# Kernel tuning notes

Measured on AMD Instinct MI355X. Metric: run time of the kernel, lower is better.

## Reference

```python
import jax, jax.numpy as jnp
import numpy as np

B, N, D, H, E, K = 8, 1024, 768, 12, 4, 9
PAD = (K - 1) // 2


def _ln(x, g, b, eps=1e-5):
    m = jnp.mean(x, -1, keepdims=True)
    v = jnp.var(x, -1, keepdims=True)
    return (x - m) * jax.lax.rsqrt(v + eps) * g + b


def setup_inputs() -> dict:
    key = jax.random.key(0)
    ks = jax.random.split(key, 12)
    w = lambda k, s: jax.random.normal(k, s, jnp.float32) * 0.02
    return {
        "x": jax.random.normal(ks[0], (B, N, D), jnp.float32),
        "ff1_ln_g": jnp.ones(D), "ff1_ln_b": jnp.zeros(D),
        "ff1_w1": w(ks[1], (D, E * D)), "ff1_b1": jnp.zeros(E * D),
        "ff1_w2": w(ks[2], (E * D, D)), "ff1_b2": jnp.zeros(D),
        "attn_ln_g": jnp.ones(D), "attn_ln_b": jnp.zeros(D),
        "qkv_w": w(ks[3], (D, 3 * D)), "qkv_b": jnp.zeros(3 * D),
        "proj_w": w(ks[4], (D, D)), "proj_b": jnp.zeros(D),
        "rel_table": w(ks[5], (2 * N - 1, H)),
        "conv_ln_g": jnp.ones(D), "conv_ln_b": jnp.zeros(D),
        "pwin_w": w(ks[6], (2 * D, D)), "pwin_b": jnp.zeros(2 * D),
        "dw_w": w(ks[7], (D, 1, K)), "dw_b": jnp.zeros(D),
        "bn_g": jnp.ones(D), "bn_b": jnp.zeros(D),
        "pwout_w": w(ks[8], (D, D)), "pwout_b": jnp.zeros(D),
        "ff2_ln_g": jnp.ones(D), "ff2_ln_b": jnp.zeros(D),
        "ff2_w1": w(ks[9], (D, E * D)), "ff2_b1": jnp.zeros(E * D),
        "ff2_w2": w(ks[10], (E * D, D)), "ff2_b2": jnp.zeros(D),
        "fin_ln_g": jnp.ones(D), "fin_ln_b": jnp.zeros(D),
    }


def _ffn(x, g, b, w1, b1, w2, b2):
    h = jax.nn.gelu(_ln(x, g, b) @ w1 + b1, approximate=False)
    return h @ w2 + b2


def _attn(x, qkv_w, qkv_b, proj_w, proj_b, rel_table):
    b_, n_, c = x.shape
    hd = c // H
    qkv = (x @ qkv_w + qkv_b).reshape(b_, n_, 3, H, hd).transpose(2, 0, 3, 1, 4)
    q, k, v = qkv[0], qkv[1], qkv[2]  # (B, H, N, hd)
    scores = jnp.einsum('bhqd,bhkd->bhqk', q, k) * (hd ** -0.5)
    coords = jnp.arange(n_)
    idx = coords[None, :] - coords[:, None] + N - 1  # (N, N) in [0, 2N-2]
    bias = rel_table[idx].transpose(2, 0, 1)  # (H, N, N)
    a = jax.nn.softmax(scores + bias[None], axis=-1)
    out = jnp.einsum('bhqk,bhkd->bhqd', a, v).transpose(0, 2, 1, 3).reshape(b_, n_, c)
    return out @ proj_w + proj_b


def _conv(x, g, b, pwin_w, pwin_b, dw_w, dw_b, bn_g, bn_b, pwout_w, pwout_b):
    y = _ln(x, g, b) @ pwin_w.T + pwin_b  # pointwise-in conv as matmul -> (B, N, 2D)
    u, gate = jnp.split(y, 2, axis=-1)
    y = (u * jax.nn.sigmoid(gate)).transpose(0, 2, 1)  # GLU over channels -> (B, D, N)
    y = jax.lax.conv_general_dilated(
        y, dw_w, (1,), [(PAD, PAD)], feature_group_count=D,
        dimension_numbers=('NCH', 'OIH', 'NCH')) + dw_b[None, :, None]
    m = jnp.mean(y, (0, 2), keepdims=True)  # BatchNorm1d, training-mode batch stats
    v = jnp.var(y, (0, 2), keepdims=True)
    y = (y - m) * jax.lax.rsqrt(v + 1e-5) * bn_g[None, :, None] + bn_b[None, :, None]
    y = y * jax.nn.sigmoid(y)  # SiLU
    y = jnp.einsum('bcn,oc->bno', y, pwout_w) + pwout_b  # pointwise-out, back to (B, N, D)
    return y


def reference(x, ff1_ln_g, ff1_ln_b, ff1_w1, ff1_b1, ff1_w2, ff1_b2,
              attn_ln_g, attn_ln_b, qkv_w, qkv_b, proj_w, proj_b, rel_table,
              conv_ln_g, conv_ln_b, pwin_w, pwin_b, dw_w, dw_b, bn_g, bn_b,
              pwout_w, pwout_b, ff2_ln_g, ff2_ln_b, ff2_w1, ff2_b1, ff2_w2, ff2_b2,
              fin_ln_g, fin_ln_b):
    x = x + 0.5 * _ffn(x, ff1_ln_g, ff1_ln_b, ff1_w1, ff1_b1, ff1_w2, ff1_b2)
    x = x + _attn(_ln(x, attn_ln_g, attn_ln_b), qkv_w, qkv_b, proj_w, proj_b, rel_table)
    x = x + _conv(x, conv_ln_g, conv_ln_b, pwin_w, pwin_b, dw_w, dw_b, bn_g, bn_b, pwout_w, pwout_b)
    x = x + 0.5 * _ffn(x, ff2_ln_g, ff2_ln_b, ff2_w1, ff2_b1, ff2_w2, ff2_b2)
    return _ln(x, fin_ln_g, fin_ln_b)
```

## Files before the change

### kernel.cpp

```cpp
#include <hip/hip_runtime.h>
#include <math.h>

#define Bb 8
#define Nn 1024
#define Dd 768
#define Hh 12
#define Mm 8192

typedef __attribute__((ext_vector_type(4))) float f32x4;
typedef __attribute__((ext_vector_type(8))) __bf16 bf16x8;

__device__ __forceinline__ float bf2f(unsigned short u) {
  union { unsigned int i; float f; } v; v.i = ((unsigned int)u) << 16; return v.f;
}
__device__ __forceinline__ unsigned short f2bf(float f) {
  union { float f; unsigned int i; } v; v.f = f;
  unsigned int u = v.i;
  return (unsigned short)((u + 0x7FFFu + ((u >> 16) & 1u)) >> 16);
}
__device__ __forceinline__ unsigned int pack2bf(float a, float b) {
  union { __bf16 h[2]; unsigned int u; } x;
  x.h[0] = (__bf16)a; x.h[1] = (__bf16)b; return x.u;
}

__device__ __forceinline__ void gload16(const void* g, void* l) {
  __builtin_amdgcn_global_load_lds(
      (const __attribute__((address_space(1))) unsigned int*)g,
      (__attribute__((address_space(3))) unsigned int*)l, 16, 0, 0);
}

template<int EPI, int NT>
__global__ __launch_bounds__(256)
void gemm_bt(const unsigned short* __restrict__ A,
             const unsigned short* __restrict__ Bt,
             const float* __restrict__ bias,
             unsigned short* __restrict__ Cbf,
             float* __restrict__ Res,
             int M, int N, int K, float scale)
{
  __shared__ __align__(16) unsigned short Asm[128*32];
  __shared__ __align__(16) unsigned short Bsm[NT*32];
  const int tid = threadIdx.x;
  const int wv = tid >> 6, lane = tid & 63;
  const int lr = lane & 15, lg = lane >> 4;
  const int wr = wv >> 1, wc = wv & 1;
  constexpr int JN = NT / 32;

  const int gx = gridDim.x, gy = gridDim.y;
  const int nwg = gx * gy;
  const int lin = blockIdx.y * gx + blockIdx.x;
  const int q8 = nwg >> 3, r8 = nwg & 7;
  const int xcd = lin & 7, lidx = lin >> 3;
  const int wg = ((xcd < r8) ? xcd * (q8 + 1) : r8 * (q8 + 1) + (xcd - r8) * q8) + lidx;
  const int bx = wg % gx;
  const int by = wg / gx;

  const int n0 = bx * NT, m0 = by * 128;

  f32x4 acc[4][JN] = {};

  const int schk = (lane & 3) * 8;
  const unsigned short* Ag = A + (size_t)(m0 + wv*32 + (lane >> 2))*K + schk;
  unsigned short* Al = Asm + wv*1024;
  const unsigned short* Bg;
  unsigned short* Bl;
  if (NT == 128) { Bg = Bt + (size_t)(n0 + wv*32 + (lane >> 2))*K + schk; Bl = Bsm + wv*1024; }
  else           { Bg = Bt + (size_t)(n0 + wv*16 + (lane >> 2))*K + schk; Bl = Bsm + wv*512; }
  const size_t rstep = (size_t)16 * K;

  for (int kt = 0; kt < K; kt += 32) {
    gload16(Ag + kt,          Al);
    gload16(Ag + kt + rstep,  Al + 512);
    gload16(Bg + kt,          Bl);
    if (NT == 128) gload16(Bg + kt + rstep, Bl + 512);
    __syncthreads();
    bf16x8 af[4], bfr[JN];
#pragma unroll
    for (int i = 0; i < 4; i++) af[i]  = *(const bf16x8*)&Asm[(wr*64 + i*16 + lr)*32 + lg*8];
#pragma unroll
    for (int j = 0; j < JN; j++) bfr[j] = *(const bf16x8*)&Bsm[(wc*(NT/2) + j*16 + lr)*32 + lg*8];
#pragma unroll
    for (int i = 0; i < 4; i++)
#pragma unroll
      for (int j = 0; j < JN; j++)
        acc[i][j] = __builtin_amdgcn_mfma_f32_16x16x32_bf16(af[i], bfr[j], acc[i][j], 0, 0, 0);
    __syncthreads();
  }

#pragma unroll
  for (int i = 0; i < 4; i++) {
    const int rg = m0 + wr*64 + i*16 + lg*4;
    if (EPI == 3) {
#pragma unroll
      for (int j = 0; j < JN; j += 2) {
        const int cgu = n0 + wc*(NT/2) + j*16 + lr;
        const float bu = bias[cgu], bg = bias[cgu + 16];
        const int ocol = (n0 >> 1) + wc*(NT/4) + (j >> 1)*16 + lr;
#pragma unroll
        for (int e = 0; e < 4; e++) {
          float u  = acc[i][j][e]   + bu;
          float gt = acc[i][j+1][e] + bg;
          Cbf[(size_t)(rg + e) * (N >> 1) + ocol] = f2bf(u / (1.f + __expf(-gt)));
        }
      }
    } else {
#pragma unroll
      for (int j = 0; j < JN; j++) {
        const int cg = n0 + wc*(NT/2) + j*16 + lr;
        const float bv = bias[cg];
#pragma unroll
        for (int e = 0; e < 4; e++) {
          float v = acc[i][j][e] + bv;
          const size_t idx = (size_t)(rg + e) * N + cg;
          if (EPI == 1) {
            v = 0.5f * v * (1.f + erff(v * 0.7071067811865475f));
            Cbf[idx] = f2bf(v);
          } else if (EPI == 0) {
            Cbf[idx] = f2bf(v);
          } else {
            Res[idx] += scale * v;
          }
        }
      }
    }
  }
}

template<bool OBF>
__global__ __launch_bounds__(256)
void ln_kernel(const float* x, const float* __restrict__ g,
               const float* __restrict__ b, void* out)
{
  const int row = blockIdx.x, tid = threadIdx.x;
  const float* xr = x + (size_t)row * Dd;
  float v0 = xr[tid], v1 = xr[tid+256], v2 = xr[tid+512];
  float s = v0+v1+v2, q = v0*v0+v1*v1+v2*v2;
  for (int off = 32; off; off >>= 1) { s += __shfl_down(s, off); q += __shfl_down(q, off); }
  __shared__ float ps[4], pq[4];
  if ((tid & 63) == 0) { ps[tid>>6] = s; pq[tid>>6] = q; }
  __syncthreads();
  s = ps[0]+ps[1]+ps[2]+ps[3]; q = pq[0]+pq[1]+pq[2]+pq[3];
  const float mean = s * (1.f/768.f);
  const float rstd = rsqrtf(q*(1.f/768.f) - mean*mean + 1e-5f);
  float y0 = (v0-mean)*rstd*g[tid]     + b[tid];
  float y1 = (v1-mean)*rstd*g[tid+256] + b[tid+256];
  float y2 = (v2-mean)*rstd*g[tid+512] + b[tid+512];
  if (OBF) {
    unsigned short* o = (unsigned short*)out + (size_t)row * Dd;
    o[tid] = f2bf(y0); o[tid+256] = f2bf(y1); o[tid+512] = f2bf(y2);
  } else {
    float* o = (float*)out + (size_t)row * Dd;
    o[tid] = y0; o[tid+256] = y1; o[tid+512] = y2;
  }
}

__global__ __launch_bounds__(256)
void transpose_w(const float* __restrict__ src, unsigned short* __restrict__ dst,
                 int K, int N)
{
  __shared__ float t[32][33];
  const int tx = threadIdx.x, ty = threadIdx.y;
  const int n0 = blockIdx.x * 32, k0 = blockIdx.y * 32;
#pragma unroll
  for (int i = 0; i < 4; i++) t[ty + i*8][tx] = src[(size_t)(k0 + ty + i*8)*N + n0 + tx];
  __syncthreads();
#pragma unroll
  for (int i = 0; i < 4; i++)
    dst[(size_t)(n0 + ty + i*8)*K + k0 + tx] = f2bf(t[tx][ty + i*8]);
}

__global__ __launch_bounds__(256)
void convert_bf(const float* __restrict__ src, unsigned short* __restrict__ dst, int n)
{
  for (int i = blockIdx.x*256 + threadIdx.x; i < n; i += gridDim.x*256)
    dst[i] = f2bf(src[i]);
}

__global__ __launch_bounds__(256)
void perm_pwin(const float* __restrict__ w, const float* __restrict__ b,
               unsigned short* __restrict__ wt, float* __restrict__ bperm)
{
  const int r = blockIdx.x;
  const int blk = r >> 7, g = (r >> 4) & 7, t = r & 15;
  const int orig = blk*64 + ((g >> 1) << 4) + t + ((g & 1) ? 768 : 0);
  const float* src = w + (size_t)orig * 768;
  unsigned short* dst = wt + (size_t)r * 768;
  const int tid = threadIdx.x;
  dst[tid] = f2bf(src[tid]); dst[tid+256] = f2bf(src[tid+256]); dst[tid+512] = f2bf(src[tid+512]);
  if (tid == 0) bperm[r] = b[orig];
}

__global__ __launch_bounds__(256)
void dw_tr(const float* __restrict__ src, float* __restrict__ dst)
{
  const int id = blockIdx.x*256 + threadIdx.x;
  if (id >= 9*768) return;
  const int k = id / 768, d = id % 768;
  dst[id] = src[d*9 + k];
}

__global__ __launch_bounds__(256)
void attn_kernel(const unsigned short* __restrict__ qkv,
                 const float* __restrict__ rel,
                 unsigned short* __restrict__ out)
{
  const int bh = blockIdx.x; const int b = bh / Hh, h = bh % Hh;
  const int q0 = blockIdx.y * 64;
  const int tid = threadIdx.x, wv = tid >> 6, lane = tid & 63;
  const int lr = lane & 15, lg = lane >> 4;

  __shared__ __align__(16) unsigned short Kl[64*72];
  __shared__ __align__(16) unsigned short Vt[64*72 + 64];
  __shared__ __align__(16) unsigned short Pl[4*16*72];
  __shared__ float relh[2048];

  for (int i = tid; i < 2047; i += 256) relh[i] = rel[(size_t)i*Hh + h];

  const size_t qrow = (size_t)(b*Nn + q0 + wv*16 + lr);
  const bf16x8 qf0 = *(const bf16x8*)(qkv + qrow*2304 + h*64 + lg*8);
  const bf16x8 qf1 = *(const bf16x8*)(qkv + qrow*2304 + h*64 + 32 + lg*8);

  const int skey = tid >> 2;
  const int sdc  = (tid & 3) * 16;
  unsigned short* Pw = Pl + wv*16*72;

  f32x4 O[4] = {};
  float mrow = -1e30f, lsum = 0.f;
  const int qq = q0 + wv*16 + lr;

  __syncthreads();

  for (int kt = 0; kt < Nn; kt += 64) {
    {
      const size_t gb = (size_t)(b*Nn + kt + skey)*2304 + h*64 + sdc;
      bf16x8 ka  = *(const bf16x8*)(qkv + gb + 768);
      bf16x8 kb8 = *(const bf16x8*)(qkv + gb + 776);
      bf16x8 va  = *(const bf16x8*)(qkv + gb + 1536);
      bf16x8 vb8 = *(const bf16x8*)(qkv + gb + 1544);
      *(bf16x8*)&Kl[skey*72 + sdc]     = ka;
      *(bf16x8*)&Kl[skey*72 + sdc + 8] = kb8;
      const unsigned short* vs = (const unsigned short*)&va;
#pragma unroll
      for (int i = 0; i < 16; i++) {
        const int d = sdc + i;
        Vt[d*72 + (d>>4)*16 + skey] = (i < 8) ? vs[i] : ((const unsigned short*)&vb8)[i-8];
      }
    }
    __syncthreads();

    f32x4 s[4] = {};
#pragma unroll
    for (int kb = 0; kb < 4; kb++) {
      bf16x8 kfa = *(const bf16x8*)&Kl[(kb*16 + lr)*72 + lg*8];
      bf16x8 kfb = *(const bf16x8*)&Kl[(kb*16 + lr)*72 + 32 + lg*8];
      s[kb] = __builtin_amdgcn_mfma_f32_16x16x32_bf16(kfa, qf0, s[kb], 0, 0, 0);
      s[kb] = __builtin_amdgcn_mfma_f32_16x16x32_bf16(kfb, qf1, s[kb], 0, 0, 0);
    }

    const int bidx = kt - qq + (Nn - 1);
    float v[4][4]; float r = -1e30f;
#pragma unroll
    for (int kb = 0; kb < 4; kb++)
#pragma unroll
      for (int j = 0; j < 4; j++) {
        float t = s[kb][j]*0.125f + relh[bidx + kb*16 + lg*4 + j];
        v[kb][j] = t; r = fmaxf(r, t);
      }
    r = fmaxf(r, __shfl_xor(r, 16)); r = fmaxf(r, __shfl_xor(r, 32));
    const float mn = fmaxf(mrow, r);
    const float al = __expf(mrow - mn);
    mrow = mn;
    float rs = 0.f;
    unsigned int pk[8];
#pragma unroll
    for (int kb = 0; kb < 4; kb++) {
      float p0 = __expf(v[kb][0]-mn), p1 = __expf(v[kb][1]-mn);
      float p2 = __expf(v[kb][2]-mn), p3 = __expf(v[kb][3]-mn);
      rs += (p0+p1) + (p2+p3);
      pk[kb*2]   = pack2bf(p0, p1);
      pk[kb*2+1] = pack2bf(p2, p3);
    }
    rs += __shfl_xor(rs, 16); rs += __shfl_xor(rs, 32);
    lsum = lsum*al + rs;

#pragma unroll
    for (int kb0 = 0; kb0 < 4; kb0++) {
      const int kb = (kb0 + lg) & 3;
      *(unsigned int*)&Pw[lr*72 + kb*16 + lg*4]     = pk[kb*2];
      *(unsigned int*)&Pw[lr*72 + kb*16 + lg*4 + 2] = pk[kb*2+1];
    }

#pragma unroll
    for (int ni = 0; ni < 4; ni++) {
      O[ni][0]*=al; O[ni][1]*=al; O[ni][2]*=al; O[ni][3]*=al;
    }

    bf16x8 pf0 = *(const bf16x8*)&Pw[lr*72 + lg*8];
    bf16x8 pf1 = *(const bf16x8*)&Pw[lr*72 + 32 + lg*8];
#pragma unroll
    for (int dt = 0; dt < 4; dt++) {
      bf16x8 vf0 = *(const bf16x8*)&Vt[(dt*16 + lr)*72 + dt*16 + lg*8];
      bf16x8 vf1 = *(const bf16x8*)&Vt[(dt*16 + lr)*72 + dt*16 + 32 + lg*8];
      O[dt] = __builtin_amdgcn_mfma_f32_16x16x32_bf16(vf0, pf0, O[dt], 0, 0, 0);
      O[dt] = __builtin_amdgcn_mfma_f32_16x16x32_bf16(vf1, pf1, O[dt], 0, 0, 0);
    }
    __syncthreads();
  }

  const float rl = 1.f / lsum;
#pragma unroll
  for (int dt = 0; dt < 4; dt++) {
    ushort4 o4;
    o4.x = f2bf(O[dt][0]*rl); o4.y = f2bf(O[dt][1]*rl);
    o4.z = f2bf(O[dt][2]*rl); o4.w = f2bf(O[dt][3]*rl);
    *(ushort4*)(out + (size_t)(b*Nn + qq)*Dd + h*64 + dt*16 + lg*4) = o4;
  }
}

__global__ __launch_bounds__(256)
void dwconv(const unsigned short* __restrict__ glu, const float* __restrict__ dwwT,
            const float* __restrict__ dwb, unsigned short* __restrict__ z)
{
  const int id = blockIdx.x*256 + threadIdx.x;
  if (id >= Mm*96) return;
  const int row = id / 96, c8 = (id % 96) * 8;
  const int n = row % Nn;
  float acc[8] = {};
#pragma unroll
  for (int k = 0; k < 9; k++) {
    const int nn = n + k - 4;
    if (nn >= 0 && nn < Nn) {
      bf16x8 gv = *(const bf16x8*)&glu[(size_t)(row + k - 4)*768 + c8];
      const float4 w0 = *(const float4*)&dwwT[k*768 + c8];
      const float4 w1 = *(const float4*)&dwwT[k*768 + c8 + 4];
      acc[0] += w0.x*(float)gv[0]; acc[1] += w0.y*(float)gv[1];
      acc[2] += w0.z*(float)gv[2]; acc[3] += w0.w*(float)gv[3];
      acc[4] += w1.x*(float)gv[4]; acc[5] += w1.y*(float)gv[5];
      acc[6] += w1.z*(float)gv[6]; acc[7] += w1.w*(float)gv[7];
    }
  }
  bf16x8 o;
#pragma unroll
  for (int e = 0; e < 8; e++) o[e] = (__bf16)(acc[e] + dwb[c8+e]);
  *(bf16x8*)&z[(size_t)row*768 + c8] = o;
}

__global__ __launch_bounds__(256)
void bn_part(const unsigned short* __restrict__ z, float* __restrict__ psum,
             float* __restrict__ psq)
{
  const int blk = blockIdx.x, tid = threadIdx.x;
  float s[3] = {0,0,0}, q[3] = {0,0,0};
  for (int r = 0; r < 128; r++) {
    const unsigned short* row = z + (size_t)(blk*128 + r) * Dd;
#pragma unroll
    for (int i = 0; i < 3; i++) { float v = bf2f(row[tid + i*256]); s[i] += v; q[i] += v*v; }
  }
#pragma unroll
  for (int i = 0; i < 3; i++) {
    psum[(size_t)blk*Dd + tid + i*256] = s[i];
    psq [(size_t)blk*Dd + tid + i*256] = q[i];
  }
}

__global__ __launch_bounds__(256)
void bn_final(const float* __restrict__ psum, const float* __restrict__ psq,
              const float* __restrict__ g, const float* __restrict__ bb,
              float* __restrict__ scale, float* __restrict__ shift)
{
  const int c = blockIdx.x*256 + threadIdx.x;
  if (c >= Dd) return;
  float s = 0.f, q = 0.f;
  for (int i = 0; i < 64; i++) { s += psum[(size_t)i*Dd + c]; q += psq[(size_t)i*Dd + c]; }
  const float mean = s / (float)Mm;
  const float var  = q / (float)Mm - mean*mean;
  const float sc = g[c] * rsqrtf(var + 1e-5f);
  scale[c] = sc; shift[c] = bb[c] - mean*sc;
}

__global__ __launch_bounds__(256)
void bn_silu(const unsigned short* __restrict__ z, const float* __restrict__ scale,
             const float* __restrict__ shift, unsigned short* __restrict__ out)
{
  const int id = blockIdx.x*256 + threadIdx.x;
  if (id >= Mm * Dd) return;
  const int c = id % Dd;
  float v = bf2f(z[id]) * scale[c] + shift[c];
  v = v / (1.f + __expf(-v));
  out[id] = f2bf(v);
}

extern "C" void kernel_launch(void* const* d_in, const int* in_sizes, int n_in,
                              void* d_out, int out_size, void* d_ws, size_t ws_size,
                              hipStream_t stream)
{
  const float* x        = (const float*)d_in[0];
  const float* ff1_ln_g = (const float*)d_in[1];
  const float* ff1_ln_b = (const float*)d_in[2];
  const float* ff1_w1   = (const float*)d_in[3];
  const float* ff1_b1   = (const float*)d_in[4];
  const float* ff1_w2   = (const float*)d_in[5];
  const float* ff1_b2   = (const float*)d_in[6];
  const float* attn_ln_g= (const float*)d_in[7];
  const float* attn_ln_b= (const float*)d_in[8];
  const float* qkv_w    = (const float*)d_in[9];
  const float* qkv_b    = (const float*)d_in[10];
  const float* proj_w   = (const float*)d_in[11];
  const float* proj_b   = (const float*)d_in[12];
  const float* rel_tab  = (const float*)d_in[13];
  const float* conv_ln_g= (const float*)d_in[14];
  const float* conv_ln_b= (const float*)d_in[15];
  const float* pwin_w   = (const float*)d_in[16];
  const float* pwin_b   = (const float*)d_in[17];
  const float* dw_w     = (const float*)d_in[18];
  const float* dw_b     = (const float*)d_in[19];
  const float* bn_g     = (const float*)d_in[20];
  const float* bn_b     = (const float*)d_in[21];
  const float* pwout_w  = (const float*)d_in[22];
  const float* pwout_b  = (const float*)d_in[23];
  const float* ff2_ln_g = (const float*)d_in[24];
  const float* ff2_ln_b = (const float*)d_in[25];
  const float* ff2_w1   = (const float*)d_in[26];
  const float* ff2_b1   = (const float*)d_in[27];
  const float* ff2_w2   = (const float*)d_in[28];
  const float* ff2_b2   = (const float*)d_in[29];
  const float* fin_ln_g = (const float*)d_in[30];
  const float* fin_ln_b = (const float*)d_in[31];

  char* ws = (char*)d_ws;
  size_t off = 0;
  auto alloc = [&](size_t bytes) { char* p = ws + off; off += (bytes + 255) & ~(size_t)255; return p; };
  unsigned short* wt_ff1_1 = (unsigned short*)alloc((size_t)3072*768*2);
  unsigned short* wt_ff1_2 = (unsigned short*)alloc((size_t)768*3072*2);
  unsigned short* wt_qkv   = (unsigned short*)alloc((size_t)2304*768*2);
  unsigned short* wt_proj  = (unsigned short*)alloc((size_t)768*768*2);
  unsigned short* wt_pwin  = (unsigned short*)alloc((size_t)1536*768*2);
  unsigned short* wt_pwout = (unsigned short*)alloc((size_t)768*768*2);
  unsigned short* wt_ff2_1 = (unsigned short*)alloc((size_t)3072*768*2);
  unsigned short* wt_ff2_2 = (unsigned short*)alloc((size_t)768*3072*2);
  unsigned short* ybf      = (unsigned short*)alloc((size_t)Mm*768*2);
  unsigned short* big      = (unsigned short*)alloc((size_t)Mm*3072*2);
  unsigned short* abuf     = (unsigned short*)alloc((size_t)Mm*768*2);
  float* psum    = (float*)alloc((size_t)64*768*4);
  float* psq     = (float*)alloc((size_t)64*768*4);
  float* bnscale = (float*)alloc((size_t)768*4);
  float* bnshift = (float*)alloc((size_t)768*4);
  float* dwwT    = (float*)alloc((size_t)9*768*4);
  float* bperm   = (float*)alloc((size_t)1536*4);
  if (off > ws_size) return;

  float* xres = (float*)d_out;
  const dim3 tb(256);

  transpose_w<<<dim3(3072/32, 768/32), dim3(32,8), 0, stream>>>(ff1_w1, wt_ff1_1, 768, 3072);
  transpose_w<<<dim3(768/32, 3072/32), dim3(32,8), 0, stream>>>(ff1_w2, wt_ff1_2, 3072, 768);
  transpose_w<<<dim3(2304/32, 768/32), dim3(32,8), 0, stream>>>(qkv_w,  wt_qkv,  768, 2304);
  transpose_w<<<dim3(768/32, 768/32),  dim3(32,8), 0, stream>>>(proj_w, wt_proj, 768, 768);
  transpose_w<<<dim3(3072/32, 768/32), dim3(32,8), 0, stream>>>(ff2_w1, wt_ff2_1, 768, 3072);
  transpose_w<<<dim3(768/32, 3072/32), dim3(32,8), 0, stream>>>(ff2_w2, wt_ff2_2, 3072, 768);
  perm_pwin<<<1536, tb, 0, stream>>>(pwin_w, pwin_b, wt_pwin, bperm);
  convert_bf<<<2048, tb, 0, stream>>>(pwout_w, wt_pwout, 768*768);
  dw_tr<<<27, tb, 0, stream>>>(dw_w, dwwT);

  hipMemcpyAsync(d_out, (const void*)x, (size_t)Mm*Dd*4, hipMemcpyDeviceToDevice, stream);

  ln_kernel<true><<<Mm, tb, 0, stream>>>(xres, ff1_ln_g, ff1_ln_b, ybf);
  gemm_bt<1,128><<<dim3(3072/128, Mm/128), tb, 0, stream>>>(ybf, wt_ff1_1, ff1_b1, big, nullptr, Mm, 3072, 768, 0.f);
  gemm_bt<2,64><<<dim3(768/64, Mm/128), tb, 0, stream>>>(big, wt_ff1_2, ff1_b2, nullptr, xres, Mm, 768, 3072, 0.5f);

  ln_kernel<true><<<Mm, tb, 0, stream>>>(xres, attn_ln_g, attn_ln_b, ybf);
  gemm_bt<0,128><<<dim3(2304/128, Mm/128), tb, 0, stream>>>(ybf, wt_qkv, qkv_b, big, nullptr, Mm, 2304, 768, 0.f);
  attn_kernel<<<dim3(Bb*Hh, Nn/64), tb, 0, stream>>>(big, rel_tab, abuf);
  gemm_bt<2,64><<<dim3(768/64, Mm/128), tb, 0, stream>>>(abuf, wt_proj, proj_b, nullptr, xres, Mm, 768, 768, 1.0f);

  ln_kernel<true><<<Mm, tb, 0, stream>>>(xres, conv_ln_g, conv_ln_b, ybf);
  gemm_bt<3,128><<<dim3(1536/128, Mm/128), tb, 0, stream>>>(ybf, wt_pwin, bperm, abuf, nullptr, Mm, 1536, 768, 0.f);
  dwconv<<<(Mm*96)/256, tb, 0, stream>>>(abuf, dwwT, dw_b, ybf);
  bn_part<<<64, tb, 0, stream>>>(ybf, psum, psq);
  bn_final<<<3, tb, 0, stream>>>(psum, psq, bn_g, bn_b, bnscale, bnshift);
  bn_silu<<<(Mm*Dd)/256, tb, 0, stream>>>(ybf, bnscale, bnshift, abuf);
  gemm_bt<2,64><<<dim3(768/64, Mm/128), tb, 0, stream>>>(abuf, wt_pwout, pwout_b, nullptr, xres, Mm, 768, 768, 1.0f);

  ln_kernel<true><<<Mm, tb, 0, stream>>>(xres, ff2_ln_g, ff2_ln_b, ybf);
  gemm_bt<1,128><<<dim3(3072/128, Mm/128), tb, 0, stream>>>(ybf, wt_ff2_1, ff2_b1, big, nullptr, Mm, 3072, 768, 0.f);
  gemm_bt<2,64><<<dim3(768/64, Mm/128), tb, 0, stream>>>(big, wt_ff2_2, ff2_b2, nullptr, xres, Mm, 768, 3072, 0.5f);

  ln_kernel<false><<<Mm, tb, 0, stream>>>(xres, fin_ln_g, fin_ln_b, (void*)xres);
}
```

Measured before the change: 636.2 us.

## Pre-transpose V, add lazy softmax rescaling, and use a fast GELU erf approximation

Three unrelated changes. A new kernel writes V transposed into scratch once, so the attention loop can fill its V tile with vector loads instead of scattered 2-byte shared-memory stores repeated by every query block. Attention now skips the running-max update and the O/lsum rescale when no row max grows by more than 8, which saves exps and multiplies at some risk of overflow margin in bf16. GELU's erff is replaced by an Abramowitz-Stegun polynomial with a hardware reciprocal, which trades exactness for cheaper epilogue math in the FFN up-projections.

```diff
diff --git a/kernel.cpp b/kernel.cpp
--- a/kernel.cpp
+++ b/kernel.cpp
@@ -27,6 +27,16 @@
   __builtin_amdgcn_global_load_lds(
       (const __attribute__((address_space(1))) unsigned int*)g,
       (__attribute__((address_space(3))) unsigned int*)l, 16, 0, 0);
+}
+
+__device__ __forceinline__ float gelu_f(float v) {
+  const float z = fabsf(v) * 0.7071067811865475f;
+  const float t = __builtin_amdgcn_rcpf(1.f + 0.3275911f * z);
+  const float poly = t*(0.254829592f + t*(-0.284496736f + t*(1.421413741f +
+                     t*(-1.453152027f + t*1.061405429f))));
+  float er = 1.f - poly * __expf(-z * z);
+  er = copysignf(er, v);
+  return 0.5f * v * (1.f + er);
 }
 
 template<int EPI, int NT>
@@ -113,8 +123,7 @@
           float v = acc[i][j][e] + bv;
           const size_t idx = (size_t)(rg + e) * N + cg;
           if (EPI == 1) {
-            v = 0.5f * v * (1.f + erff(v * 0.7071067811865475f));
-            Cbf[idx] = f2bf(v);
+            Cbf[idx] = f2bf(gelu_f(v));
           } else if (EPI == 0) {
             Cbf[idx] = f2bf(v);
           } else {
@@ -200,7 +209,32 @@
 }
 
 __global__ __launch_bounds__(256)
+void v_transpose(const unsigned short* __restrict__ big, unsigned short* __restrict__ vtr)
+{
+  __shared__ unsigned short t[64][72];
+  const int bh = blockIdx.x;
+  const int b = bh / Hh, h = bh % Hh;
+  const int n0 = blockIdx.y * 64;
+  const int tid = threadIdx.x;
+  const int r = tid >> 2, cc = (tid & 3) * 16;
+  const size_t gb = (size_t)(b*Nn + n0 + r)*2304 + 1536 + h*64 + cc;
+  *(bf16x8*)&t[r][cc]     = *(const bf16x8*)(big + gb);
+  *(bf16x8*)&t[r][cc + 8] = *(const bf16x8*)(big + gb + 8);
+  __syncthreads();
+  const int d = tid >> 2, nn = (tid & 3) * 16;
+  bf16x8 o0, o1;
+#pragma unroll
+  for (int i = 0; i < 8; i++) o0[i] = *(const __bf16*)&t[nn + i][d];
+#pragma unroll
+  for (int i = 0; i < 8; i++) o1[i] = *(const __bf16*)&t[nn + 8 + i][d];
+  unsigned short* dst = vtr + ((size_t)bh*64 + d)*Nn + n0 + nn;
+  *(bf16x8*)dst = o0;
+  *(bf16x8*)(dst + 8) = o1;
+}
+
+__global__ __launch_bounds__(256)
 void attn_kernel(const unsigned short* __restrict__ qkv,
+                 const unsigned short* __restrict__ vtr,
                  const float* __restrict__ rel,
                  unsigned short* __restrict__ out)
 {
@@ -220,8 +254,8 @@
   const bf16x8 qf0 = *(const bf16x8*)(qkv + qrow*2304 + h*64 + lg*8);
   const bf16x8 qf1 = *(const bf16x8*)(qkv + qrow*2304 + h*64 + 32 + lg*8);
 
-  const int skey = tid >> 2;
-  const int sdc  = (tid & 3) * 16;
+  const int sd = tid >> 2;
+  const int sc = (tid & 3) * 16;
   unsigned short* Pw = Pl + wv*16*72;
 
   f32x4 O[4] = {};
@@ -232,19 +266,13 @@
 
   for (int kt = 0; kt < Nn; kt += 64) {
     {
-      const size_t gb = (size_t)(b*Nn + kt + skey)*2304 + h*64 + sdc;
-      bf16x8 ka  = *(const bf16x8*)(qkv + gb + 768);
-      bf16x8 kb8 = *(const bf16x8*)(qkv + gb + 776);
-      bf16x8 va  = *(const bf16x8*)(qkv + gb + 1536);
-      bf16x8 vb8 = *(const bf16x8*)(qkv + gb + 1544);
-      *(bf16x8*)&Kl[skey*72 + sdc]     = ka;
-      *(bf16x8*)&Kl[skey*72 + sdc + 8] = kb8;
-      const unsigned short* vs = (const unsigned short*)&va;
-#pragma unroll
-      for (int i = 0; i < 16; i++) {
-        const int d = sdc + i;
-        Vt[d*72 + (d>>4)*16 + skey] = (i < 8) ? vs[i] : ((const unsigned short*)&vb8)[i-8];
-      }
+      const size_t gk = (size_t)(b*Nn + kt + sd)*2304 + 768 + h*64 + sc;
+      *(bf16x8*)&Kl[sd*72 + sc]     = *(const bf16x8*)(qkv + gk);
+      *(bf16x8*)&Kl[sd*72 + sc + 8] = *(const bf16x8*)(qkv + gk + 8);
+      const size_t gv = ((size_t)bh*64 + sd)*Nn + kt + sc;
+      const int vb = sd*72 + (sd>>4)*16 + sc;
+      *(bf16x8*)&Vt[vb]     = *(const bf16x8*)(vtr + gv);
+      *(bf16x8*)&Vt[vb + 8] = *(const bf16x8*)(vtr + gv + 8);
     }
     __syncthreads();
 
@@ -267,32 +295,36 @@
         v[kb][j] = t; r = fmaxf(r, t);
       }
     r = fmaxf(r, __shfl_xor(r, 16)); r = fmaxf(r, __shfl_xor(r, 32));
-    const float mn = fmaxf(mrow, r);
-    const float al = __expf(mrow - mn);
-    mrow = mn;
+
+    if (!__all(r <= mrow + 8.f)) {
+      const float mn = fmaxf(mrow, r);
+      const float al = __expf(mrow - mn);
+      mrow = mn;
+      lsum *= al;
+#pragma unroll
+      for (int ni = 0; ni < 4; ni++) {
+        O[ni][0]*=al; O[ni][1]*=al; O[ni][2]*=al; O[ni][3]*=al;
+      }
+    }
+
     float rs = 0.f;
     unsigned int pk[8];
 #pragma unroll
     for (int kb = 0; kb < 4; kb++) {
-      float p0 = __expf(v[kb][0]-mn), p1 = __expf(v[kb][1]-mn);
-      float p2 = __expf(v[kb][2]-mn), p3 = __expf(v[kb][3]-mn);
+      float p0 = __expf(v[kb][0]-mrow), p1 = __expf(v[kb][1]-mrow);
+      float p2 = __expf(v[kb][2]-mrow), p3 = __expf(v[kb][3]-mrow);
       rs += (p0+p1) + (p2+p3);
       pk[kb*2]   = pack2bf(p0, p1);
       pk[kb*2+1] = pack2bf(p2, p3);
     }
     rs += __shfl_xor(rs, 16); rs += __shfl_xor(rs, 32);
-    lsum = lsum*al + rs;
+    lsum += rs;
 
 #pragma unroll
     for (int kb0 = 0; kb0 < 4; kb0++) {
       const int kb = (kb0 + lg) & 3;
       *(unsigned int*)&Pw[lr*72 + kb*16 + lg*4]     = pk[kb*2];
       *(unsigned int*)&Pw[lr*72 + kb*16 + lg*4 + 2] = pk[kb*2+1];
-    }
-
-#pragma unroll
-    for (int ni = 0; ni < 4; ni++) {
-      O[ni][0]*=al; O[ni][1]*=al; O[ni][2]*=al; O[ni][3]*=al;
     }
 
     bf16x8 pf0 = *(const bf16x8*)&Pw[lr*72 + lg*8];
@@ -449,6 +481,8 @@
   float* bperm   = (float*)alloc((size_t)1536*4);
   if (off > ws_size) return;
 
+  unsigned short* vtr = ybf;
+
   float* xres = (float*)d_out;
   const dim3 tb(256);
 
@@ -470,7 +504,8 @@
 
   ln_kernel<true><<<Mm, tb, 0, stream>>>(xres, attn_ln_g, attn_ln_b, ybf);
   gemm_bt<0,128><<<dim3(2304/128, Mm/128), tb, 0, stream>>>(ybf, wt_qkv, qkv_b, big, nullptr, Mm, 2304, 768, 0.f);
-  attn_kernel<<<dim3(Bb*Hh, Nn/64), tb, 0, stream>>>(big, rel_tab, abuf);
+  v_transpose<<<dim3(Bb*Hh, Nn/64), tb, 0, stream>>>(big, vtr);
+  attn_kernel<<<dim3(Bb*Hh, Nn/64), tb, 0, stream>>>(big, vtr, rel_tab, abuf);
   gemm_bt<2,64><<<dim3(768/64, Mm/128), tb, 0, stream>>>(abuf, wt_proj, proj_b, nullptr, xres, Mm, 768, 768, 1.0f);
 
   ln_kernel<true><<<Mm, tb, 0, stream>>>(xres, conv_ln_g, conv_ln_b, ybf);
```

Result: no change. 645.0 us (+1.4%).
